# Kernel optimization log

Measured on AMD Instinct MI355X. Metric: run time of the kernel, lower is better.

Reference implementation:

```python
import jax, jax.numpy as jnp
import numpy as np

GROUP_SIZE = 128  # vLLM machete default group size
ZERO_POINT = 8.0  # uint4b8: stored unsigned 4-bit, logical value = q - 8


def setup_inputs() -> dict:
    key = jax.random.key(0)
    k_a, k_b, k_s = jax.random.split(key, 3)
    M, K, N = 4096, 4096, 12288
    a = jax.random.normal(k_a, (M, K), dtype=jnp.float32)
    # int4 quantized weights stored as small ints in [0, 16)
    b_q = jax.random.randint(k_b, (K, N), 0, 16, dtype=jnp.int32)
    # per-group scales: one scale per (group of 128 rows of K) per output column
    scales = jax.random.uniform(k_s, (K // GROUP_SIZE, N), dtype=jnp.float32) * 0.02 + 0.001
    return {"a": a, "b_q": b_q, "scales": scales}


def reference(a, b_q, scales):
    K, N = b_q.shape
    G = K // GROUP_SIZE
    # dequantize: (q - 8) * group_scale, scale broadcast over each K-group
    b = (b_q.astype(jnp.float32) - ZERO_POINT).reshape(G, GROUP_SIZE, N)
    b = (b * scales[:, None, :]).reshape(K, N)  # [K, N] dequantized weights
    return a @ b  # [M, N]
```

## Files before the change

### kernel.cpp

```cpp
#include <hip/hip_runtime.h>
#include <hip/hip_bf16.h>
#include <stdint.h>

constexpr int Mdim = 4096;
constexpr int Kdim = 4096;
constexpr int Ndim = 12288;

constexpr int TILE_M = 128;
constexpr int TILE_N = 128;
constexpr int TILE_K = 64;
constexpr int NKT = Kdim / TILE_K;
constexpr int GRID_M = Mdim / TILE_M;
constexpr int GRID_N = Ndim / TILE_N;
constexpr int NWG = GRID_M * GRID_N;

typedef float  f32x4   __attribute__((ext_vector_type(4)));
typedef __bf16 bf16x4v __attribute__((ext_vector_type(4)));
typedef __bf16 bf16x8v __attribute__((ext_vector_type(8)));
typedef int    i32x4   __attribute__((ext_vector_type(4)));
typedef unsigned short ushort8 __attribute__((ext_vector_type(8)));

typedef __attribute__((address_space(3))) uint32_t       lds_u32;
typedef __attribute__((address_space(1))) const uint32_t glb_u32;

__device__ __forceinline__ void gload16(const void* g, void* l) {
    __builtin_amdgcn_global_load_lds((glb_u32*)(uintptr_t)g,
                                     (lds_u32*)(uint32_t)(uintptr_t)l, 16, 0, 0);
}

__launch_bounds__(256)
__global__ void cvtA(const float* __restrict__ A, unsigned short* __restrict__ Aw) {
    int t = blockIdx.x * 256 + threadIdx.x;
    int r = t >> 9;
    int c = t & 511;
    const float* src = A + ((long)r << 12) + (c << 3);
    f32x4 v0 = *(const f32x4*)src;
    f32x4 v1 = *(const f32x4*)(src + 4);
    bf16x8v o;
#pragma unroll
    for (int j = 0; j < 4; ++j) { o[j] = (__bf16)v0[j]; o[4 + j] = (__bf16)v1[j]; }
    int cs = (c & ~7) | ((c ^ r) & 7);
    *(bf16x8v*)(Aw + ((long)r << 12) + (cs << 3)) = o;
}

__launch_bounds__(256)
__global__ void deqB(const int* __restrict__ Bq, const float* __restrict__ S,
                     unsigned short* __restrict__ Bw) {
    __shared__ unsigned short lt[64][72];
    int kb = blockIdx.x & 63;
    int nb = blockIdx.x >> 6;
    int k0 = kb << 6, n0 = nb << 6;
    int tid = threadIdx.x;
    int g = k0 >> 7;
    int nq = (tid & 15) << 2;
    f32x4 sc = *(const f32x4*)(S + (long)g * Ndim + n0 + nq);
#pragma unroll
    for (int p = 0; p < 4; ++p) {
        int kk = (p << 4) + (tid >> 4);
        i32x4 q = *(const i32x4*)(Bq + (long)(k0 + kk) * Ndim + n0 + nq);
#pragma unroll
        for (int j = 0; j < 4; ++j) {
            float v = ((float)q[j] - 8.f) * sc[j];
            lt[nq + j][kk] = __builtin_bit_cast(unsigned short, (__bf16)v);
        }
    }
    __syncthreads();
#pragma unroll
    for (int h = 0; h < 2; ++h) {
        int cidx = tid + (h << 8);
        int n = cidx >> 3, s = cidx & 7;
        int sp = s ^ (n & 7);
        ushort8 v = *(const ushort8*)&lt[n][s << 3];
        *(ushort8*)(Bw + (long)(n0 + n) * Kdim + k0 + (sp << 3)) = v;
    }
}

__launch_bounds__(256, 3)
__global__ void gemm_bf16(const unsigned short* __restrict__ Aw,
                          const unsigned short* __restrict__ Bw,
                          float* __restrict__ C) {
    __shared__ unsigned char sA[TILE_M * TILE_K * 2];
    __shared__ unsigned char sB[TILE_N * TILE_K * 2];

    const int tid  = threadIdx.x;
    const int lane = tid & 63;
    const int w    = tid >> 6;

    const int bid   = blockIdx.x;
    const int x     = bid & 7;
    const int local = bid >> 3;
    const int pn    = local >> 5;
    const int tm    = local & 31;
    const int tn    = x * 12 + pn;
    const int brow  = tm << 7;
    const int bcol  = tn << 7;

    const unsigned char* ga[4];
    const unsigned char* gb[4];
#pragma unroll
    for (int i = 0; i < 4; ++i) {
        int c = (w << 8) + (i << 6) + lane;
        int r = c >> 3, s = c & 7;
        ga[i] = (const unsigned char*)Aw + (long)(brow + r) * (Kdim * 2) + (s << 4);
        gb[i] = (const unsigned char*)Bw + (long)(bcol + r) * (Kdim * 2) + (s << 4);
    }

    const int fr = lane & 15;
    const int ks = lane >> 4;
    const int wr = w >> 1, wc = w & 1;
    int ra[4][2], rb[4][2];
#pragma unroll
    for (int m = 0; m < 4; ++m)
#pragma unroll
        for (int kk = 0; kk < 2; ++kk) {
            int r_a = wr * 64 + m * 16 + fr;
            int r_b = wc * 64 + m * 16 + fr;
            ra[m][kk] = (r_a << 7) + ((((kk << 2) + ks) ^ (r_a & 7)) << 4);
            rb[m][kk] = (r_b << 7) + ((((kk << 2) + ks) ^ (r_b & 7)) << 4);
        }

    f32x4 acc[4][4];
#pragma unroll
    for (int m = 0; m < 4; ++m)
#pragma unroll
        for (int n = 0; n < 4; ++n) acc[m][n] = (f32x4){0.f, 0.f, 0.f, 0.f};

    for (int kt = 0; kt < NKT; ++kt) {
#pragma unroll
        for (int i = 0; i < 4; ++i) {
            gload16(ga[i], sA + (((w << 2) + i) << 10));
            gload16(gb[i], sB + (((w << 2) + i) << 10));
            ga[i] += TILE_K * 2;
            gb[i] += TILE_K * 2;
        }
        __syncthreads();

#pragma unroll
        for (int kk = 0; kk < 2; ++kk) {
            bf16x8v af[4], bf[4];
#pragma unroll
            for (int m = 0; m < 4; ++m) af[m] = *(const bf16x8v*)(sA + ra[m][kk]);
#pragma unroll
            for (int n = 0; n < 4; ++n) bf[n] = *(const bf16x8v*)(sB + rb[n][kk]);
#pragma unroll
            for (int m = 0; m < 4; ++m)
#pragma unroll
                for (int n = 0; n < 4; ++n)
                    acc[m][n] = __builtin_amdgcn_mfma_f32_16x16x32_bf16(af[m], bf[n], acc[m][n], 0, 0, 0);
        }
        __syncthreads();
    }

#pragma unroll
    for (int m = 0; m < 4; ++m) {
        int row = brow + wr * 64 + m * 16 + ks * 4;
#pragma unroll
        for (int n = 0; n < 4; ++n) {
            int col = bcol + wc * 64 + n * 16 + fr;
            f32x4 v = acc[m][n];
            float* cp = C + (long)row * Ndim + col;
#pragma unroll
            for (int r = 0; r < 4; ++r) cp[(long)r * Ndim] = v[r];
        }
    }
}

__device__ __forceinline__ int swz_f(int row, int kbyte) {
    int s = kbyte >> 4;
    int f = s ^ ((row ^ (row >> 2)) & 7);
    return (row << 7) + (f << 4) + (kbyte & 15);
}

__launch_bounds__(256, 2)
__global__ void machete_fused(const float* __restrict__ A,
                              const int* __restrict__ Bq,
                              const float* __restrict__ S,
                              float* __restrict__ C) {
    __shared__ unsigned char sA[TILE_M * TILE_K * 2];
    __shared__ unsigned char sB[TILE_N * TILE_K * 2];

    const int tid = threadIdx.x;
    const int bid = blockIdx.x;
    const int sid = (bid & 7) * (NWG / 8) + (bid >> 3);
    const int tm = sid / GRID_N;
    const int tn = sid % GRID_N;
    const int brow = tm * TILE_M;
    const int bcol = tn * TILE_N;

    const int a_row0 = tid >> 4;
    const int a_kb   = tid & 15;
    const int b_kb = tid >> 4;
    const int b_nb = tid & 15;

    int aw[8];
#pragma unroll
    for (int i = 0; i < 8; ++i) aw[i] = swz_f(a_row0 + 16 * i, a_kb * 8);
    int bw[2][4];
#pragma unroll
    for (int i = 0; i < 2; ++i)
#pragma unroll
        for (int j = 0; j < 4; ++j) bw[i][j] = swz_f(4 * b_nb + 64 * i + j, b_kb * 8);

    const int lane = tid & 63;
    const int w  = tid >> 6;
    const int wr = w >> 1, wc = w & 1;
    const int fr = lane & 15;
    const int ks = lane >> 4;
    int ar[4][2], br[4][2];
#pragma unroll
    for (int m = 0; m < 4; ++m)
#pragma unroll
        for (int kk = 0; kk < 2; ++kk) {
            ar[m][kk] = swz_f(wr * 64 + m * 16 + fr, kk * 64 + ks * 16);
            br[m][kk] = swz_f(wc * 64 + m * 16 + fr, kk * 64 + ks * 16);
        }

    const float* Ap = A + (long)brow * Kdim;
    const int*   Bp = Bq + bcol;

    f32x4 aregs[8];
    i32x4 bregs[2][4];
    f32x4 sregs[2];

#pragma unroll
    for (int i = 0; i < 8; ++i)
        aregs[i] = *(const f32x4*)(Ap + (long)(a_row0 + 16 * i) * Kdim + a_kb * 4);
#pragma unroll
    for (int i = 0; i < 2; ++i) {
#pragma unroll
        for (int r = 0; r < 4; ++r)
            bregs[i][r] = *(const i32x4*)(Bp + (long)(b_kb * 4 + r) * Ndim + 4 * b_nb + 64 * i);
        sregs[i] = *(const f32x4*)(S + bcol + 4 * b_nb + 64 * i);
    }

    f32x4 acc[4][4];
#pragma unroll
    for (int m = 0; m < 4; ++m)
#pragma unroll
        for (int n = 0; n < 4; ++n) acc[m][n] = (f32x4){0.f, 0.f, 0.f, 0.f};

    for (int kt = 0; kt < NKT; ++kt) {
#pragma unroll
        for (int i = 0; i < 8; ++i) {
            f32x4 v = aregs[i];
            bf16x4v p;
            p[0] = (__bf16)v[0]; p[1] = (__bf16)v[1];
            p[2] = (__bf16)v[2]; p[3] = (__bf16)v[3];
            *(bf16x4v*)(sA + aw[i]) = p;
        }
#pragma unroll
        for (int i = 0; i < 2; ++i) {
            f32x4 sc = sregs[i];
#pragma unroll
            for (int j = 0; j < 4; ++j) {
                float scj = sc[j];
                float nm8 = -8.f * scj;
                bf16x4v p;
#pragma unroll
                for (int r = 0; r < 4; ++r) {
                    float v = (float)bregs[i][r][j] * scj + nm8;
                    p[r] = (__bf16)v;
                }
                *(bf16x4v*)(sB + bw[i][j]) = p;
            }
        }
        __syncthreads();

        if (kt + 1 < NKT) {
            const float* Ap2 = Ap + (kt + 1) * TILE_K;
            const int*   Bp2 = Bp + (long)((kt + 1) * TILE_K) * Ndim;
            const float* Sp2 = S + (long)((kt + 1) >> 1) * Ndim + bcol;
#pragma unroll
            for (int i = 0; i < 8; ++i)
                aregs[i] = *(const f32x4*)(Ap2 + (long)(a_row0 + 16 * i) * Kdim + a_kb * 4);
#pragma unroll
            for (int i = 0; i < 2; ++i) {
#pragma unroll
                for (int r = 0; r < 4; ++r)
                    bregs[i][r] = *(const i32x4*)(Bp2 + (long)(b_kb * 4 + r) * Ndim + 4 * b_nb + 64 * i);
                sregs[i] = *(const f32x4*)(Sp2 + 4 * b_nb + 64 * i);
            }
        }

#pragma unroll
        for (int kk = 0; kk < 2; ++kk) {
            bf16x8v af[4], bfv[4];
#pragma unroll
            for (int m = 0; m < 4; ++m) af[m] = *(const bf16x8v*)(sA + ar[m][kk]);
#pragma unroll
            for (int n = 0; n < 4; ++n) bfv[n] = *(const bf16x8v*)(sB + br[n][kk]);
#pragma unroll
            for (int m = 0; m < 4; ++m)
#pragma unroll
                for (int n = 0; n < 4; ++n)
                    acc[m][n] = __builtin_amdgcn_mfma_f32_16x16x32_bf16(af[m], bfv[n], acc[m][n], 0, 0, 0);
        }
        __syncthreads();
    }

#pragma unroll
    for (int m = 0; m < 4; ++m) {
        int row = brow + wr * 64 + m * 16 + ks * 4;
#pragma unroll
        for (int n = 0; n < 4; ++n) {
            int col = bcol + wc * 64 + n * 16 + fr;
            f32x4 v = acc[m][n];
            float* cp = C + (long)row * Ndim + col;
#pragma unroll
            for (int r = 0; r < 4; ++r) cp[(long)r * Ndim] = v[r];
        }
    }
}

extern "C" void kernel_launch(void* const* d_in, const int* in_sizes, int n_in,
                              void* d_out, int out_size, void* d_ws, size_t ws_size,
                              hipStream_t stream) {
    const float* A  = (const float*)d_in[0];
    const int*   Bq = (const int*)d_in[1];
    const float* S  = (const float*)d_in[2];
    float* C = (float*)d_out;

    const size_t a_elems = (size_t)Mdim * Kdim;
    const size_t b_elems = (size_t)Ndim * Kdim;
    const size_t need = (a_elems + b_elems) * sizeof(unsigned short);

    if (ws_size >= need) {
        unsigned short* Aw = (unsigned short*)d_ws;
        unsigned short* Bw = Aw + a_elems;
        hipLaunchKernelGGL(cvtA, dim3((Mdim * Kdim / 8) / 256), dim3(256), 0, stream, A, Aw);
        hipLaunchKernelGGL(deqB, dim3((Kdim / 64) * (Ndim / 64)), dim3(256), 0, stream, Bq, S, Bw);
        hipLaunchKernelGGL(gemm_bf16, dim3(NWG), dim3(256), 0, stream, Aw, Bw, C);
    } else {
        hipLaunchKernelGGL(machete_fused, dim3(NWG), dim3(256), 0, stream, A, Bq, S, C);
    }
}
```

Before: 562.8 us.

## Add 256x256 double-buffered 8-wave bf16 GEMM with interleaved prefetch and new swizzle

Adds a new GEMM kernel with 256x256 tiles, 512 threads and 128KB of dynamic LDS. It double-buffers K tiles, prefetches half-tiles between MFMA phases, and raises wave priority around the MFMA blocks. The A/B staging layout moves to two 32-element K halves with a 4-way XOR swizzle, and cvtA, deqB and the fallback gemm are updated to match. The goal is more data reuse per tile and overlap of global loads with compute, at the cost of heavy register and LDS use and a dependence on the dynamic shared memory attribute call succeeding.

New measurement: 469.0 us. 16.7% less time.

```diff
diff --git a/kernel.cpp b/kernel.cpp
--- a/kernel.cpp
+++ b/kernel.cpp
@@ -6,12 +6,12 @@
 constexpr int Kdim = 4096;
 constexpr int Ndim = 12288;
 
-constexpr int TILE_M = 128;
-constexpr int TILE_N = 128;
-constexpr int TILE_K = 64;
-constexpr int NKT = Kdim / TILE_K;
-constexpr int GRID_M = Mdim / TILE_M;
-constexpr int GRID_N = Ndim / TILE_N;
+constexpr int NKT = Kdim / 64;
+constexpr int GM256 = Mdim / 256;
+constexpr int GN256 = Ndim / 256;
+constexpr int NWG256 = GM256 * GN256;
+constexpr int GRID_M = Mdim / 128;
+constexpr int GRID_N = Ndim / 128;
 constexpr int NWG = GRID_M * GRID_N;
 
 typedef float  f32x4   __attribute__((ext_vector_type(4)));
@@ -27,6 +27,7 @@
     __builtin_amdgcn_global_load_lds((glb_u32*)(uintptr_t)g,
                                      (lds_u32*)(uint32_t)(uintptr_t)l, 16, 0, 0);
 }
+
 
 __launch_bounds__(256)
 __global__ void cvtA(const float* __restrict__ A, unsigned short* __restrict__ Aw) {
@@ -39,8 +40,9 @@
     bf16x8v o;
 #pragma unroll
     for (int j = 0; j < 4; ++j) { o[j] = (__bf16)v0[j]; o[4 + j] = (__bf16)v1[j]; }
-    int cs = (c & ~7) | ((c ^ r) & 7);
-    *(bf16x8v*)(Aw + ((long)r << 12) + (cs << 3)) = o;
+    int ks = c & 3;
+    int cp = (c & ~3) | (ks ^ ((r >> 1) & 3));
+    *(bf16x8v*)(Aw + ((long)r << 12) + (cp << 3)) = o;
 }
 
 __launch_bounds__(256)
@@ -68,10 +70,159 @@
 #pragma unroll
     for (int h = 0; h < 2; ++h) {
         int cidx = tid + (h << 8);
-        int n = cidx >> 3, s = cidx & 7;
-        int sp = s ^ (n & 7);
-        ushort8 v = *(const ushort8*)&lt[n][s << 3];
-        *(ushort8*)(Bw + (long)(n0 + n) * Kdim + k0 + (sp << 3)) = v;
+        int n = cidx >> 3, sidx = cidx & 7;
+        int kh = sidx >> 2, ks = sidx & 3;
+        int ksp = ks ^ ((n >> 1) & 3);
+        ushort8 v = *(const ushort8*)&lt[n][sidx << 3];
+        *(ushort8*)(Bw + (long)(n0 + n) * Kdim + k0 + kh * 32 + ksp * 8) = v;
+    }
+}
+
+__launch_bounds__(512, 2)
+__global__ void gemm256(const unsigned short* __restrict__ Aw,
+                        const unsigned short* __restrict__ Bw,
+                        float* __restrict__ C) {
+    extern __shared__ unsigned char ldsbuf[];
+
+    const int tid  = threadIdx.x;
+    const int lane = tid & 63;
+    const int w    = tid >> 6;
+    const int wr   = w >> 2, wc = w & 3;
+    const int fr   = lane & 15;
+    const int ks   = lane >> 4;
+
+    const int bid = blockIdx.x;
+    const int xcd = bid & 7;
+    const int loc = bid >> 3;
+    const int pn  = loc >> 4;
+    const int tm  = loc & 15;
+    const int tn  = xcd * 6 + pn;
+    const int brow = tm << 8, bcol = tn << 8;
+
+    const unsigned char* baseA = (const unsigned char*)Aw
+        + (size_t)(brow + (tid >> 2)) * 8192 + (size_t)(tid & 3) * 16;
+    const unsigned char* baseB = (const unsigned char*)Bw
+        + (size_t)(bcol + (tid >> 2)) * 8192 + (size_t)(tid & 3) * 16;
+
+    int offA[8][2], offB[4][2];
+#pragma unroll
+    for (int am = 0; am < 8; ++am)
+#pragma unroll
+        for (int kh = 0; kh < 2; ++kh) {
+            int rowL = wr * 128 + am * 16 + fr;
+            offA[am][kh] = (kh << 14) + rowL * 64 + ((ks ^ ((rowL >> 1) & 3)) << 4);
+        }
+#pragma unroll
+    for (int n = 0; n < 4; ++n)
+#pragma unroll
+        for (int kh = 0; kh < 2; ++kh) {
+            int colL = wc * 64 + n * 16 + fr;
+            offB[n][kh] = (kh << 14) + colL * 64 + ((ks ^ ((colL >> 1) & 3)) << 4);
+        }
+
+    auto stageA = [&](int tile, int kh) {
+        if (tile < NKT) {
+            const unsigned char* s = baseA + (size_t)tile * 128 + (kh << 6);
+            unsigned char* d = ldsbuf + ((tile & 1) << 16) + (kh << 14) + (w << 10);
+            gload16(s, d);
+            gload16(s + 1048576, d + 8192);
+        }
+    };
+    auto stageB = [&](int tile, int kh) {
+        if (tile < NKT) {
+            const unsigned char* s = baseB + (size_t)tile * 128 + (kh << 6);
+            unsigned char* d = ldsbuf + ((tile & 1) << 16) + 32768 + (kh << 14) + (w << 10);
+            gload16(s, d);
+            gload16(s + 1048576, d + 8192);
+        }
+    };
+
+    f32x4 acc[8][4];
+#pragma unroll
+    for (int m = 0; m < 8; ++m)
+#pragma unroll
+        for (int n = 0; n < 4; ++n) acc[m][n] = (f32x4){0.f, 0.f, 0.f, 0.f};
+
+    stageA(0, 0); stageB(0, 0); stageA(0, 1); stageB(0, 1);
+    stageA(1, 0); stageB(1, 0);
+    asm volatile("s_waitcnt vmcnt(4)" ::: "memory");
+    __builtin_amdgcn_s_barrier();
+
+    for (int T = 0; T < NKT; ++T) {
+        unsigned char* sAc = ldsbuf + ((T & 1) << 16);
+        unsigned char* sBc = sAc + 32768;
+        bf16x8v bA[4], aF[4];
+
+#pragma unroll
+        for (int n = 0; n < 4; ++n) bA[n] = *(const bf16x8v*)(sBc + offB[n][0]);
+#pragma unroll
+        for (int m = 0; m < 4; ++m) aF[m] = *(const bf16x8v*)(sAc + offA[m][0]);
+        stageA(T + 1, 1);
+        __builtin_amdgcn_s_barrier();
+        __builtin_amdgcn_s_setprio(1);
+#pragma unroll
+        for (int m = 0; m < 4; ++m)
+#pragma unroll
+            for (int n = 0; n < 4; ++n)
+                acc[m][n] = __builtin_amdgcn_mfma_f32_16x16x32_bf16(aF[m], bA[n], acc[m][n], 0, 0, 0);
+        __builtin_amdgcn_s_setprio(0);
+        __builtin_amdgcn_s_barrier();
+
+#pragma unroll
+        for (int m = 0; m < 4; ++m) aF[m] = *(const bf16x8v*)(sAc + offA[4 + m][0]);
+        stageB(T + 1, 1);
+        __builtin_amdgcn_s_barrier();
+        __builtin_amdgcn_s_setprio(1);
+#pragma unroll
+        for (int m = 0; m < 4; ++m)
+#pragma unroll
+            for (int n = 0; n < 4; ++n)
+                acc[4 + m][n] = __builtin_amdgcn_mfma_f32_16x16x32_bf16(aF[m], bA[n], acc[4 + m][n], 0, 0, 0);
+        __builtin_amdgcn_s_setprio(0);
+        __builtin_amdgcn_s_barrier();
+
+#pragma unroll
+        for (int n = 0; n < 4; ++n) bA[n] = *(const bf16x8v*)(sBc + offB[n][1]);
+#pragma unroll
+        for (int m = 0; m < 4; ++m) aF[m] = *(const bf16x8v*)(sAc + offA[m][1]);
+        stageA(T + 2, 0);
+        __builtin_amdgcn_s_barrier();
+        __builtin_amdgcn_s_setprio(1);
+#pragma unroll
+        for (int m = 0; m < 4; ++m)
+#pragma unroll
+            for (int n = 0; n < 4; ++n)
+                acc[m][n] = __builtin_amdgcn_mfma_f32_16x16x32_bf16(aF[m], bA[n], acc[m][n], 0, 0, 0);
+        __builtin_amdgcn_s_setprio(0);
+        __builtin_amdgcn_s_barrier();
+
+#pragma unroll
+        for (int m = 0; m < 4; ++m) aF[m] = *(const bf16x8v*)(sAc + offA[4 + m][1]);
+        stageB(T + 2, 0);
+        __builtin_amdgcn_s_barrier();
+        __builtin_amdgcn_s_setprio(1);
+#pragma unroll
+        for (int m = 0; m < 4; ++m)
+#pragma unroll
+            for (int n = 0; n < 4; ++n)
+                acc[4 + m][n] = __builtin_amdgcn_mfma_f32_16x16x32_bf16(aF[m], bA[n], acc[4 + m][n], 0, 0, 0);
+        __builtin_amdgcn_s_setprio(0);
+        if (T < NKT - 2) asm volatile("s_waitcnt vmcnt(4)" ::: "memory");
+        else             asm volatile("s_waitcnt vmcnt(0)" ::: "memory");
+        __builtin_amdgcn_s_barrier();
+    }
+
+#pragma unroll
+    for (int am = 0; am < 8; ++am) {
+        int row = brow + wr * 128 + am * 16 + ks * 4;
+#pragma unroll
+        for (int n = 0; n < 4; ++n) {
+            int col = bcol + wc * 64 + n * 16 + fr;
+            f32x4 v = acc[am][n];
+            float* cp = C + (long)row * Ndim + col;
+#pragma unroll
+            for (int r = 0; r < 4; ++r) cp[(long)r * Ndim] = v[r];
+        }
     }
 }
 
@@ -79,8 +230,8 @@
 __global__ void gemm_bf16(const unsigned short* __restrict__ Aw,
                           const unsigned short* __restrict__ Bw,
                           float* __restrict__ C) {
-    __shared__ unsigned char sA[TILE_M * TILE_K * 2];
-    __shared__ unsigned char sB[TILE_N * TILE_K * 2];
+    __shared__ unsigned char sA[128 * 64 * 2];
+    __shared__ unsigned char sB[128 * 64 * 2];
 
     const int tid  = threadIdx.x;
     const int lane = tid & 63;
@@ -101,8 +252,8 @@
     for (int i = 0; i < 4; ++i) {
         int c = (w << 8) + (i << 6) + lane;
         int r = c >> 3, s = c & 7;
-        ga[i] = (const unsigned char*)Aw + (long)(brow + r) * (Kdim * 2) + (s << 4);
-        gb[i] = (const unsigned char*)Bw + (long)(bcol + r) * (Kdim * 2) + (s << 4);
+        ga[i] = (const unsigned char*)Aw + (long)(brow + r) * 8192 + (s << 4);
+        gb[i] = (const unsigned char*)Bw + (long)(bcol + r) * 8192 + (s << 4);
     }
 
     const int fr = lane & 15;
@@ -115,8 +266,8 @@
         for (int kk = 0; kk < 2; ++kk) {
             int r_a = wr * 64 + m * 16 + fr;
             int r_b = wc * 64 + m * 16 + fr;
-            ra[m][kk] = (r_a << 7) + ((((kk << 2) + ks) ^ (r_a & 7)) << 4);
-            rb[m][kk] = (r_b << 7) + ((((kk << 2) + ks) ^ (r_b & 7)) << 4);
+            ra[m][kk] = (r_a << 7) + (kk << 6) + ((ks ^ ((r_a >> 1) & 3)) << 4);
+            rb[m][kk] = (r_b << 7) + (kk << 6) + ((ks ^ ((r_b >> 1) & 3)) << 4);
         }
 
     f32x4 acc[4][4];
@@ -130,8 +281,8 @@
         for (int i = 0; i < 4; ++i) {
             gload16(ga[i], sA + (((w << 2) + i) << 10));
             gload16(gb[i], sB + (((w << 2) + i) << 10));
-            ga[i] += TILE_K * 2;
-            gb[i] += TILE_K * 2;
+            ga[i] += 128;
+            gb[i] += 128;
         }
         __syncthreads();
 
@@ -176,16 +327,16 @@
                               const int* __restrict__ Bq,
                               const float* __restrict__ S,
                               float* __restrict__ C) {
-    __shared__ unsigned char sA[TILE_M * TILE_K * 2];
-    __shared__ unsigned char sB[TILE_N * TILE_K * 2];
+    __shared__ unsigned char sA[128 * 64 * 2];
+    __shared__ unsigned char sB[128 * 64 * 2];
 
     const int tid = threadIdx.x;
     const int bid = blockIdx.x;
     const int sid = (bid & 7) * (NWG / 8) + (bid >> 3);
     const int tm = sid / GRID_N;
     const int tn = sid % GRID_N;
-    const int brow = tm * TILE_M;
-    const int bcol = tn * TILE_N;
+    const int brow = tm * 128;
+    const int bcol = tn * 128;
 
     const int a_row0 = tid >> 4;
     const int a_kb   = tid & 15;
@@ -267,8 +418,8 @@
         __syncthreads();
 
         if (kt + 1 < NKT) {
-            const float* Ap2 = Ap + (kt + 1) * TILE_K;
-            const int*   Bp2 = Bp + (long)((kt + 1) * TILE_K) * Ndim;
+            const float* Ap2 = Ap + (kt + 1) * 64;
+            const int*   Bp2 = Bq + bcol + (long)((kt + 1) * 64) * Ndim;
             const float* Sp2 = S + (long)((kt + 1) >> 1) * Ndim + bcol;
 #pragma unroll
             for (int i = 0; i < 8; ++i)
@@ -329,7 +480,14 @@
         unsigned short* Bw = Aw + a_elems;
         hipLaunchKernelGGL(cvtA, dim3((Mdim * Kdim / 8) / 256), dim3(256), 0, stream, A, Aw);
         hipLaunchKernelGGL(deqB, dim3((Kdim / 64) * (Ndim / 64)), dim3(256), 0, stream, Bq, S, Bw);
-        hipLaunchKernelGGL(gemm_bf16, dim3(NWG), dim3(256), 0, stream, Aw, Bw, C);
+        hipError_t e = hipFuncSetAttribute(
+            reinterpret_cast<const void*>(gemm256),
+            hipFuncAttributeMaxDynamicSharedMemorySize, 131072);
+        if (e == hipSuccess) {
+            hipLaunchKernelGGL(gemm256, dim3(NWG256), dim3(512), 131072, stream, Aw, Bw, C);
+        } else {
+            hipLaunchKernelGGL(gemm_bf16, dim3(NWG), dim3(256), 0, stream, Aw, Bw, C);
+        }
     } else {
         hipLaunchKernelGGL(machete_fused, dim3(NWG), dim3(256), 0, stream, A, Bq, S, C);
     }
```

## Add triple-buffered 256x128 bf16 GEMM with barrier-scheduled prefetch and new swizzle

Applied to the files above, without the earlier changes.

Adds a new GEMM kernel with 256x128 output tiles per workgroup, a three-stage LDS ring buffer in dynamic shared memory (72 KB), and async global-to-LDS prefetch two K-steps ahead. The K loop is split into half-steps with explicit barriers, setprio around MFMA blocks, and manual vmcnt waits to overlap loads with compute. The pre-pass A and B layouts switch to a 64-byte-row XOR swizzle to match the new LDS layout. This larger tile raises arithmetic intensity and hides memory latency, at the cost of more registers (8x4 accumulators), lower occupancy, and fragile hand-scheduled synchronisation.

After: 517.5 us. 1.09x faster.

```diff
diff --git a/kernel.cpp b/kernel.cpp
--- a/kernel.cpp
+++ b/kernel.cpp
@@ -6,12 +6,12 @@
 constexpr int Kdim = 4096;
 constexpr int Ndim = 12288;
 
-constexpr int TILE_M = 128;
-constexpr int TILE_N = 128;
-constexpr int TILE_K = 64;
-constexpr int NKT = Kdim / TILE_K;
-constexpr int GRID_M = Mdim / TILE_M;
-constexpr int GRID_N = Ndim / TILE_N;
+constexpr int NKT = Kdim / 64;
+constexpr int GM = Mdim / 256;
+constexpr int GN = Ndim / 128;
+constexpr int NWGP = GM * GN;
+constexpr int GRID_M = Mdim / 128;
+constexpr int GRID_N = Ndim / 128;
 constexpr int NWG = GRID_M * GRID_N;
 
 typedef float  f32x4   __attribute__((ext_vector_type(4)));
@@ -27,6 +27,7 @@
     __builtin_amdgcn_global_load_lds((glb_u32*)(uintptr_t)g,
                                      (lds_u32*)(uint32_t)(uintptr_t)l, 16, 0, 0);
 }
+
 
 __launch_bounds__(256)
 __global__ void cvtA(const float* __restrict__ A, unsigned short* __restrict__ Aw) {
@@ -39,8 +40,9 @@
     bf16x8v o;
 #pragma unroll
     for (int j = 0; j < 4; ++j) { o[j] = (__bf16)v0[j]; o[4 + j] = (__bf16)v1[j]; }
-    int cs = (c & ~7) | ((c ^ r) & 7);
-    *(bf16x8v*)(Aw + ((long)r << 12) + (cs << 3)) = o;
+    int ks = c & 3;
+    int cp = (c & ~3) | (ks ^ ((r >> 1) & 3));
+    *(bf16x8v*)(Aw + ((long)r << 12) + (cp << 3)) = o;
 }
 
 __launch_bounds__(256)
@@ -68,19 +70,152 @@
 #pragma unroll
     for (int h = 0; h < 2; ++h) {
         int cidx = tid + (h << 8);
-        int n = cidx >> 3, s = cidx & 7;
-        int sp = s ^ (n & 7);
-        ushort8 v = *(const ushort8*)&lt[n][s << 3];
-        *(ushort8*)(Bw + (long)(n0 + n) * Kdim + k0 + (sp << 3)) = v;
-    }
+        int n = cidx >> 3, sidx = cidx & 7;
+        int kh = sidx >> 2, ks = sidx & 3;
+        int ksp = ks ^ ((n >> 1) & 3);
+        ushort8 v = *(const ushort8*)&lt[n][sidx << 3];
+        *(ushort8*)(Bw + (long)(n0 + n) * Kdim + k0 + kh * 32 + ksp * 8) = v;
+    }
+}
+
+__launch_bounds__(256, 2)
+__global__ void gemm_p(const unsigned short* __restrict__ Aw,
+                       const unsigned short* __restrict__ Bw,
+                       float* __restrict__ C) {
+    extern __shared__ unsigned char lds[];
+
+    const int tid  = threadIdx.x;
+    const int lane = tid & 63;
+    const int w    = tid >> 6;
+    const int wr   = w >> 1, wc = w & 1;
+    const int fr   = lane & 15;
+    const int ks   = lane >> 4;
+
+    const int bid = blockIdx.x;
+    const int xcd = bid & 7;
+    const int loc = bid >> 3;
+    const int pn  = loc >> 4;
+    const int tm  = loc & 15;
+    const int tn  = xcd * 12 + pn;
+    const int brow = tm << 8, bcol = tn << 7;
+
+    const unsigned char* pa0 = (const unsigned char*)Aw
+        + (size_t)(brow + (tid >> 2)) * 8192 + (size_t)(tid & 3) * 16;
+    const unsigned char* pa1 = pa0 + (size_t)64 * 8192;
+    const unsigned char* pa2 = pa0 + (size_t)128 * 8192;
+    const unsigned char* pa3 = pa0 + (size_t)192 * 8192;
+    const unsigned char* pb0 = (const unsigned char*)Bw
+        + (size_t)(bcol + (tid >> 2)) * 8192 + (size_t)(tid & 3) * 16;
+    const unsigned char* pb1 = pb0 + (size_t)64 * 8192;
+    const int ldw = w << 10;
+
+    int offA[8], offB[4];
+#pragma unroll
+    for (int m = 0; m < 8; ++m) {
+        int rA = wr * 128 + m * 16 + fr;
+        offA[m] = rA * 64 + ((ks ^ ((rA >> 1) & 3)) << 4);
+    }
+#pragma unroll
+    for (int n = 0; n < 4; ++n) {
+        int cB = wc * 64 + n * 16 + fr;
+        offB[n] = 16384 + cB * 64 + ((ks ^ ((cB >> 1) & 3)) << 4);
+    }
+
+    f32x4 acc[8][4];
+#pragma unroll
+    for (int m = 0; m < 8; ++m)
+#pragma unroll
+        for (int n = 0; n < 4; ++n) acc[m][n] = (f32x4){0.f, 0.f, 0.f, 0.f};
+
+#define STAGEA(R, OFF)                                                        \
+    gload16(pa0 + (OFF), lds + (R) * 24576 + 0 * 4096 + ldw);                 \
+    gload16(pa1 + (OFF), lds + (R) * 24576 + 1 * 4096 + ldw);                 \
+    gload16(pa2 + (OFF), lds + (R) * 24576 + 2 * 4096 + ldw);                 \
+    gload16(pa3 + (OFF), lds + (R) * 24576 + 3 * 4096 + ldw);
+#define STAGEB(R, OFF)                                                        \
+    gload16(pb0 + (OFF), lds + (R) * 24576 + 16384 + 0 * 4096 + ldw);         \
+    gload16(pb1 + (OFF), lds + (R) * 24576 + 16384 + 1 * 4096 + ldw);
+
+#define RD(R, off) (*(const bf16x8v*)(lds + (R) * 24576 + (off)))
+
+#define HSTEP(R, J, STG, VM)                                                  \
+    {                                                                         \
+        bf16x8v a[8], b[4];                                                   \
+        _Pragma("unroll") for (int m = 0; m < 4; ++m) a[m] = RD(R, offA[m]);  \
+        _Pragma("unroll") for (int n = 0; n < 4; ++n) b[n] = RD(R, offB[n]);  \
+        if (STG) { STAGEA(((R) + 2) % 3, ((J) + 2) * 64) }                    \
+        __builtin_amdgcn_s_barrier();                                         \
+        __builtin_amdgcn_s_setprio(1);                                        \
+        _Pragma("unroll") for (int m = 0; m < 4; ++m)                         \
+            _Pragma("unroll") for (int n = 0; n < 4; ++n)                     \
+                acc[m][n] = __builtin_amdgcn_mfma_f32_16x16x32_bf16(          \
+                    a[m], b[n], acc[m][n], 0, 0, 0);                          \
+        __builtin_amdgcn_s_setprio(0);                                        \
+        __builtin_amdgcn_s_barrier();                                         \
+        _Pragma("unroll") for (int m = 4; m < 8; ++m) a[m] = RD(R, offA[m]);  \
+        if (STG) { STAGEB(((R) + 2) % 3, ((J) + 2) * 64) }                    \
+        __builtin_amdgcn_s_barrier();                                         \
+        __builtin_amdgcn_s_setprio(1);                                        \
+        _Pragma("unroll") for (int m = 4; m < 8; ++m)                         \
+            _Pragma("unroll") for (int n = 0; n < 4; ++n)                     \
+                acc[m][n] = __builtin_amdgcn_mfma_f32_16x16x32_bf16(          \
+                    a[m], b[n], acc[m][n], 0, 0, 0);                          \
+        __builtin_amdgcn_s_setprio(0);                                        \
+        asm volatile("s_waitcnt vmcnt(" #VM ")" ::: "memory");                \
+        __builtin_amdgcn_s_barrier();                                         \
+    }
+
+    STAGEA(0, 0) STAGEB(0, 0)
+    STAGEA(1, 64) STAGEB(1, 64)
+    asm volatile("s_waitcnt vmcnt(6)" ::: "memory");
+    __builtin_amdgcn_s_barrier();
+
+    for (int it = 0; it < 42; ++it) {
+        HSTEP(0, 0, 1, 6)
+        HSTEP(1, 1, 1, 6)
+        HSTEP(2, 2, 1, 6)
+        pa0 += 192; pa1 += 192; pa2 += 192; pa3 += 192;
+        pb0 += 192; pb1 += 192;
+    }
+    HSTEP(0, 0, 0, 0)
+    {
+        bf16x8v a[8], b[4];
+#pragma unroll
+        for (int m = 0; m < 8; ++m) a[m] = RD(1, offA[m]);
+#pragma unroll
+        for (int n = 0; n < 4; ++n) b[n] = RD(1, offB[n]);
+#pragma unroll
+        for (int m = 0; m < 8; ++m)
+#pragma unroll
+            for (int n = 0; n < 4; ++n)
+                acc[m][n] = __builtin_amdgcn_mfma_f32_16x16x32_bf16(
+                    a[m], b[n], acc[m][n], 0, 0, 0);
+    }
+
+#pragma unroll
+    for (int m = 0; m < 8; ++m) {
+        int row = brow + wr * 128 + m * 16 + ks * 4;
+#pragma unroll
+        for (int n = 0; n < 4; ++n) {
+            int col = bcol + wc * 64 + n * 16 + fr;
+            f32x4 v = acc[m][n];
+            float* cp = C + (size_t)row * Ndim + col;
+#pragma unroll
+            for (int r = 0; r < 4; ++r) cp[(size_t)r * Ndim] = v[r];
+        }
+    }
+#undef HSTEP
+#undef RD
+#undef STAGEB
+#undef STAGEA
 }
 
 __launch_bounds__(256, 3)
 __global__ void gemm_bf16(const unsigned short* __restrict__ Aw,
                           const unsigned short* __restrict__ Bw,
                           float* __restrict__ C) {
-    __shared__ unsigned char sA[TILE_M * TILE_K * 2];
-    __shared__ unsigned char sB[TILE_N * TILE_K * 2];
+    __shared__ unsigned char sA[128 * 64 * 2];
+    __shared__ unsigned char sB[128 * 64 * 2];
 
     const int tid  = threadIdx.x;
     const int lane = tid & 63;
@@ -101,8 +236,8 @@
     for (int i = 0; i < 4; ++i) {
         int c = (w << 8) + (i << 6) + lane;
         int r = c >> 3, s = c & 7;
-        ga[i] = (const unsigned char*)Aw + (long)(brow + r) * (Kdim * 2) + (s << 4);
-        gb[i] = (const unsigned char*)Bw + (long)(bcol + r) * (Kdim * 2) + (s << 4);
+        ga[i] = (const unsigned char*)Aw + (long)(brow + r) * 8192 + (s << 4);
+        gb[i] = (const unsigned char*)Bw + (long)(bcol + r) * 8192 + (s << 4);
     }
 
     const int fr = lane & 15;
@@ -115,8 +250,8 @@
         for (int kk = 0; kk < 2; ++kk) {
             int r_a = wr * 64 + m * 16 + fr;
             int r_b = wc * 64 + m * 16 + fr;
-            ra[m][kk] = (r_a << 7) + ((((kk << 2) + ks) ^ (r_a & 7)) << 4);
-            rb[m][kk] = (r_b << 7) + ((((kk << 2) + ks) ^ (r_b & 7)) << 4);
+            ra[m][kk] = (r_a << 7) + (kk << 6) + ((ks ^ ((r_a >> 1) & 3)) << 4);
+            rb[m][kk] = (r_b << 7) + (kk << 6) + ((ks ^ ((r_b >> 1) & 3)) << 4);
         }
 
     f32x4 acc[4][4];
@@ -130,8 +265,8 @@
         for (int i = 0; i < 4; ++i) {
             gload16(ga[i], sA + (((w << 2) + i) << 10));
             gload16(gb[i], sB + (((w << 2) + i) << 10));
-            ga[i] += TILE_K * 2;
-            gb[i] += TILE_K * 2;
+            ga[i] += 128;
+            gb[i] += 128;
         }
         __syncthreads();
 
@@ -176,16 +311,16 @@
                               const int* __restrict__ Bq,
                               const float* __restrict__ S,
                               float* __restrict__ C) {
-    __shared__ unsigned char sA[TILE_M * TILE_K * 2];
-    __shared__ unsigned char sB[TILE_N * TILE_K * 2];
+    __shared__ unsigned char sA[128 * 64 * 2];
+    __shared__ unsigned char sB[128 * 64 * 2];
 
     const int tid = threadIdx.x;
     const int bid = blockIdx.x;
     const int sid = (bid & 7) * (NWG / 8) + (bid >> 3);
     const int tm = sid / GRID_N;
     const int tn = sid % GRID_N;
-    const int brow = tm * TILE_M;
-    const int bcol = tn * TILE_N;
+    const int brow = tm * 128;
+    const int bcol = tn * 128;
 
     const int a_row0 = tid >> 4;
     const int a_kb   = tid & 15;
@@ -267,8 +402,8 @@
         __syncthreads();
 
         if (kt + 1 < NKT) {
-            const float* Ap2 = Ap + (kt + 1) * TILE_K;
-            const int*   Bp2 = Bp + (long)((kt + 1) * TILE_K) * Ndim;
+            const float* Ap2 = Ap + (kt + 1) * 64;
+            const int*   Bp2 = Bq + bcol + (long)((kt + 1) * 64) * Ndim;
             const float* Sp2 = S + (long)((kt + 1) >> 1) * Ndim + bcol;
 #pragma unroll
             for (int i = 0; i < 8; ++i)
@@ -329,7 +464,14 @@
         unsigned short* Bw = Aw + a_elems;
         hipLaunchKernelGGL(cvtA, dim3((Mdim * Kdim / 8) / 256), dim3(256), 0, stream, A, Aw);
         hipLaunchKernelGGL(deqB, dim3((Kdim / 64) * (Ndim / 64)), dim3(256), 0, stream, Bq, S, Bw);
-        hipLaunchKernelGGL(gemm_bf16, dim3(NWG), dim3(256), 0, stream, Aw, Bw, C);
+        hipError_t e = hipFuncSetAttribute(
+            reinterpret_cast<const void*>(gemm_p),
+            hipFuncAttributeMaxDynamicSharedMemorySize, 73728);
+        if (e == hipSuccess) {
+            hipLaunchKernelGGL(gemm_p, dim3(NWGP), dim3(256), 73728, stream, Aw, Bw, C);
+        } else {
+            hipLaunchKernelGGL(gemm_bf16, dim3(NWG), dim3(256), 0, stream, Aw, Bw, C);
+        }
     } else {
         hipLaunchKernelGGL(machete_fused, dim3(NWG), dim3(256), 0, stream, A, Bq, S, C);
     }
```
